# Kernel optimization log

Measured on AMD Instinct MI355X. Metric: run time of the kernel, lower is better.

Reference implementation:

```python
import jax, jax.numpy as jnp
import numpy as np

WS = (2, 7, 7)          # window size (Wd, Wh, Ww)
SS = (1, 3, 3)          # shift size
DIM = 96
HEADS = 3
HD = DIM // HEADS       # head dim = 32
N = WS[0] * WS[1] * WS[2]  # 98 tokens per window
EPS = 1e-5


def _rel_index():
    c = np.stack(np.meshgrid(np.arange(WS[0]), np.arange(WS[1]), np.arange(WS[2]), indexing='ij')).reshape(3, -1)
    r = (c[:, :, None] - c[:, None, :]).transpose(1, 2, 0)  # (N, N, 3)
    r[..., 0] += WS[0] - 1
    r[..., 1] += WS[1] - 1
    r[..., 2] += WS[2] - 1
    r[..., 0] *= (2 * WS[1] - 1) * (2 * WS[2] - 1)
    r[..., 1] *= 2 * WS[2] - 1
    return jnp.asarray(r.sum(-1))  # (N, N) int

REL_IDX = _rel_index()


def _ln(x, w, b):
    m = x.mean(-1, keepdims=True)
    v = ((x - m) ** 2).mean(-1, keepdims=True)
    return (x - m) * jax.lax.rsqrt(v + EPS) * w + b


def setup_inputs() -> dict:
    key = jax.random.key(0)
    ks = jax.random.split(key, 10)
    B, D, H, W, C = 2, 16, 112, 112, DIM
    nW = (D // WS[0]) * (H // WS[1]) * (W // WS[2])  # 2048
    s = 0.02
    tbl = (2 * WS[0] - 1) * (2 * WS[1] - 1) * (2 * WS[2] - 1)
    return dict(
        x=jax.random.normal(ks[0], (B, D, H, W, C), jnp.float32),
        mask=jax.random.normal(ks[1], (nW, N, N), jnp.float32),
        norm1_w=jnp.ones((C,), jnp.float32), norm1_b=jnp.zeros((C,), jnp.float32),
        qkv_w=jax.random.normal(ks[2], (C, 3 * C), jnp.float32) * s,
        qkv_b=jnp.zeros((3 * C,), jnp.float32),
        rpb_table=jax.random.normal(ks[3], (tbl, HEADS), jnp.float32) * s,
        proj_w=jax.random.normal(ks[4], (C, C), jnp.float32) * s,
        proj_b=jnp.zeros((C,), jnp.float32),
        norm2_w=jnp.ones((C,), jnp.float32), norm2_b=jnp.zeros((C,), jnp.float32),
        fc1_w=jax.random.normal(ks[5], (C, 4 * C), jnp.float32) * s,
        fc1_b=jnp.zeros((4 * C,), jnp.float32),
        fc2_w=jax.random.normal(ks[6], (4 * C, C), jnp.float32) * s,
        fc2_b=jnp.zeros((C,), jnp.float32),
    )


def reference(x, mask, norm1_w, norm1_b, qkv_w, qkv_b, rpb_table, proj_w, proj_b,
              norm2_w, norm2_b, fc1_w, fc1_b, fc2_w, fc2_b):
    B, D, H, W, C = x.shape
    shortcut = x
    x = _ln(x, norm1_w, norm1_b)
    # shift (dims divisible by window -> no padding needed)
    x = jnp.roll(x, shift=(-SS[0], -SS[1], -SS[2]), axis=(1, 2, 3))
    nd, nh, nw = D // WS[0], H // WS[1], W // WS[2]
    # window partition -> (B*nW, N, C)
    xw = x.reshape(B, nd, WS[0], nh, WS[1], nw, WS[2], C)
    xw = xw.transpose(0, 1, 3, 5, 2, 4, 6, 7).reshape(-1, N, C)
    B_ = xw.shape[0]
    qkv = (xw @ qkv_w + qkv_b).reshape(B_, N, 3, HEADS, HD).transpose(2, 0, 3, 1, 4)
    q, k, v = qkv[0] * (HD ** -0.5), qkv[1], qkv[2]
    attn = jnp.einsum('bhnd,bhmd->bhnm', q, k)  # (B_, H, N, N)
    bias = rpb_table[REL_IDX.reshape(-1)].reshape(N, N, HEADS).transpose(2, 0, 1)
    attn = attn + bias[None]
    nWm = mask.shape[0]
    attn = attn.reshape(B_ // nWm, nWm, HEADS, N, N) + mask[None, :, None]
    attn = jax.nn.softmax(attn.reshape(B_, HEADS, N, N), axis=-1)
    out = jnp.einsum('bhnm,bhmd->bhnd', attn, v).transpose(0, 2, 1, 3).reshape(B_, N, C)
    out = out @ proj_w + proj_b
    # window reverse
    x = out.reshape(B, nd, nh, nw, WS[0], WS[1], WS[2], C)
    x = x.transpose(0, 1, 4, 2, 5, 3, 6, 7).reshape(B, D, H, W, C)
    x = jnp.roll(x, shift=SS, axis=(1, 2, 3))
    x = shortcut + x
    y = _ln(x, norm2_w, norm2_b)
    y = jax.nn.gelu(y @ fc1_w + fc1_b, approximate=False) @ fc2_w + fc2_b
    return x + y
```

## Files before the change

### kernel.cpp

```cpp
#include <hip/hip_runtime.h>

typedef float f32x4 __attribute__((ext_vector_type(4)));
typedef __bf16 bf16x8 __attribute__((ext_vector_type(8)));
typedef unsigned short ushort_t;
typedef ushort_t us4 __attribute__((ext_vector_type(4)));
typedef unsigned int u32x4 __attribute__((ext_vector_type(4)));

#define MFMA16(a, b, c) __builtin_amdgcn_mfma_f32_16x16x32_bf16((a), (b), (c), 0, 0, 0)

__device__ __forceinline__ ushort_t f2bf(float f) {
    unsigned int u = __builtin_bit_cast(unsigned int, f);
    u += 0x7fffu + ((u >> 16) & 1u);
    return (ushort_t)(u >> 16);
}
__device__ __forceinline__ float bf2f(ushort_t u) {
    return __builtin_bit_cast(float, (unsigned int)u << 16);
}
__device__ __forceinline__ unsigned int packbf2(float lo, float hi) {
    return ((unsigned int)f2bf(hi) << 16) | (unsigned int)f2bf(lo);
}

__device__ __forceinline__ float gelu_fast(float x) {
    float x2 = x * x;
    float t = __builtin_fmaf(0.044715f * x2, x, x);
    float e = __builtin_amdgcn_exp2f(t * (-1.5957691216f * 1.44269504f));
    return x * __builtin_amdgcn_rcpf(1.0f + e);
}

#define NTOK 98
#define CCH 96
#define QSCALE 0.17677669529663687f

#define WQKVP_OFF   ((size_t)0)
#define WPROJP_OFF  (WQKVP_OFF + (size_t)27648 * 2)
#define WFC1P_OFF   (WPROJP_OFF + (size_t)9216 * 2)
#define WFC2P_OFF   (WFC1P_OFF + (size_t)36864 * 2)
#define BIAS2_OFF   (WFC2P_OFF + (size_t)36864 * 2)
#define MASK2_OFF   (BIAS2_OFF + (size_t)37632 * 2 + 256)

__global__ __launch_bounds__(256) void prep_kernel(
    const float* __restrict__ qkv_w, const float* __restrict__ proj_w,
    const float* __restrict__ fc1_w, const float* __restrict__ fc2_w,
    const float* __restrict__ rpb,
    ushort_t* __restrict__ wqkvP, ushort_t* __restrict__ wprojP,
    ushort_t* __restrict__ wfc1P, ushort_t* __restrict__ wfc2P,
    ushort_t* __restrict__ bias2)
{
    int i = blockIdx.x * 256 + threadIdx.x;
    if (i < 27648) {
        int f = i >> 9, r = i & 511, lane = r >> 3, m = r & 7;
        int k0 = f % 3, t = f / 3, nt = t % 2, t2 = t / 2, w = t2 % 3, h = t2 / 3;
        int row = k0 * 32 + (lane >> 4) * 8 + m;
        int col = w * 96 + h * 32 + nt * 16 + (lane & 15);
        wqkvP[i] = f2bf(qkv_w[row * 288 + col]);
        return;
    }
    i -= 27648;
    if (i < 9216) {
        int f = i >> 9, r = i & 511, lane = r >> 3, m = r & 7;
        int k0 = f % 3, nt = f / 3;
        int row = k0 * 32 + (lane >> 4) * 8 + m;
        int col = nt * 16 + (lane & 15);
        wprojP[i] = f2bf(proj_w[row * 96 + col]);
        return;
    }
    i -= 9216;
    if (i < 36864) {
        int f = i >> 9, r = i & 511, lane = r >> 3, m = r & 7;
        int k0 = f % 3, nt = f / 3;
        int row = k0 * 32 + (lane >> 4) * 8 + m;
        int col = nt * 16 + (lane & 15);
        wfc1P[i] = f2bf(fc1_w[row * 384 + col]);
        return;
    }
    i -= 36864;
    if (i < 36864) {
        int f = i >> 9, r = i & 511, lane = r >> 3, m = r & 7;
        int k0 = f % 12, nt = f / 12;
        int row = k0 * 32 + (lane >> 4) * 8 + m;
        int col = nt * 16 + (lane & 15);
        wfc2P[i] = f2bf(fc2_w[row * 96 + col]);
        return;
    }
    i -= 36864;
    if (i < 37632) {
        int h = i / 12544, rem = i % 12544;
        int mt = rem / 1792, rem2 = rem % 1792, kc = rem2 >> 4, r16 = rem2 & 15;
        int row = mt * 16 + r16;
        float v = 0.f;
        if (row < 98 && kc < 98) {
            int rd = row / 49 - kc / 49 + 1;
            int rh = (row % 49) / 7 - (kc % 49) / 7 + 6;
            int rw = row % 7 - kc % 7 + 6;
            v = rpb[((rd * 13 + rh) * 13 + rw) * 3 + h];
        }
        bias2[i] = f2bf(v);
    }
}

__global__ __launch_bounds__(256) void mask2_kernel(
    const float* __restrict__ mask, ushort_t* __restrict__ mask2)
{
    __shared__ float m_lds[9604];
    const int wm = blockIdx.x;
    const float* mw = mask + (size_t)wm * 9604;
    for (int i = threadIdx.x; i < 9604; i += 256) m_lds[i] = mw[i];
    __syncthreads();
    ushort_t* out = mask2 + (size_t)wm * 12544;
    for (int g = threadIdx.x; g < 3136; g += 256) {
        int mt = g / 448, rem = g % 448, kc = rem >> 2, r4 = (rem & 3) * 4;
        us4 o;
        #pragma unroll
        for (int e = 0; e < 4; ++e) {
            int row = mt * 16 + r4 + e;
            float v = (row < 98 && kc < 98) ? m_lds[row * 98 + kc] : -1e30f;
            o[e] = f2bf(v);
        }
        *(us4*)(out + (size_t)g * 4) = o;
    }
}

__global__ __launch_bounds__(192, 3) void fused_attn(
    const float* __restrict__ x, const ushort_t* __restrict__ mask2,
    const float* __restrict__ n1w, const float* __restrict__ n1b,
    const float* __restrict__ qkv_b, const float* __restrict__ proj_b,
    const ushort_t* __restrict__ wqkvP, const ushort_t* __restrict__ wprojP,
    const ushort_t* __restrict__ bias2, float* __restrict__ dout)
{
    __shared__ ushort_t xw_lds[112 * 104];
    __shared__ ushort_t sc_all[3][2176];
    __shared__ int tokbase[112];

    const int tid  = threadIdx.x;
    const int lane = tid & 63;
    const int wave = tid >> 6;
    const int l16  = lane & 15, lg = lane >> 4;

    const int b  = blockIdx.x;
    const int wm = (b & 7) * 256 + ((b >> 3) >> 1);
    const int bb = (b >> 3) & 1;
    const int id_ = wm >> 8, ih = (wm >> 4) & 15, iw = wm & 15;

    if (tid < 98) {
        int td = tid / 49, r49 = tid - td * 49, th = r49 / 7, tw = r49 - th * 7;
        int od = (id_ * 2 + td + 1) & 15;
        int oh = ih * 7 + th + 3; if (oh >= 112) oh -= 112;
        int ow = iw * 7 + tw + 3; if (ow >= 112) ow -= 112;
        tokbase[tid] = ((((bb << 4) + od) * 112 + oh) * 112 + ow) * 96;
    }
    {
        us4 z4 = {0, 0, 0, 0};
        for (int i = tid; i < 14 * 26; i += 192) {
            int t = 98 + i / 26, c4 = (i % 26) * 4;
            *(us4*)(xw_lds + t * 104 + c4) = z4;
        }
    }
    __syncthreads();

    {
        const int g = tid >> 5, lane32 = tid & 31;
        for (int t = g; t < 98; t += 6) {
            const float* xp = x + tokbase[t];
            float v0 = xp[lane32], v1 = xp[lane32 + 32], v2 = xp[lane32 + 64];
            float s = v0 + v1 + v2, sq = v0 * v0 + v1 * v1 + v2 * v2;
            #pragma unroll
            for (int m = 1; m < 32; m <<= 1) { s += __shfl_xor(s, m); sq += __shfl_xor(sq, m); }
            float mean = s * (1.0f / 96.0f);
            float var = sq * (1.0f / 96.0f) - mean * mean;
            float rs = rsqrtf(var + 1e-5f);
            ushort_t* op = xw_lds + t * 104;
            op[lane32]      = f2bf((v0 - mean) * rs * n1w[lane32]      + n1b[lane32]);
            op[lane32 + 32] = f2bf((v1 - mean) * rs * n1w[lane32 + 32] + n1b[lane32 + 32]);
            op[lane32 + 64] = f2bf((v2 - mean) * rs * n1w[lane32 + 64] + n1b[lane32 + 64]);
        }
    }
    __syncthreads();

    const int h = wave;
    ushort_t* sc = sc_all[wave];
    const ushort_t* m2w = mask2 + (size_t)wm * 12544;
    const ushort_t* b2h = bias2 + (size_t)h * 12544;

    bf16x8 qf[7], kf[7], vf[2][4];

    #pragma unroll
    for (int which = 0; which < 2; ++which) {
        bf16x8 bw[2][3];
        float  bia[2];
        #pragma unroll
        for (int nt = 0; nt < 2; ++nt) {
            bia[nt] = qkv_b[which * 96 + h * 32 + nt * 16 + l16];
            #pragma unroll
            for (int k0 = 0; k0 < 3; ++k0)
                bw[nt][k0] = *(const bf16x8*)(wqkvP + ((((h * 3 + which) * 2 + nt) * 3 + k0) << 9) + lane * 8);
        }
        for (int mt = 0; mt < 7; ++mt) {
            const ushort_t* ap = xw_lds + (mt * 16 + l16) * 104 + lg * 8;
            bf16x8 a0 = *(const bf16x8*)(ap);
            bf16x8 a1 = *(const bf16x8*)(ap + 32);
            bf16x8 a2 = *(const bf16x8*)(ap + 64);
            #pragma unroll
            for (int nt = 0; nt < 2; ++nt) {
                f32x4 acc = {0.f, 0.f, 0.f, 0.f};
                acc = MFMA16(a0, bw[nt][0], acc);
                acc = MFMA16(a1, bw[nt][1], acc);
                acc = MFMA16(a2, bw[nt][2], acc);
                float scl = (which == 0) ? QSCALE : 1.0f;
                #pragma unroll
                for (int j = 0; j < 4; ++j)
                    sc[(lg * 4 + j) * 36 + nt * 16 + l16] = f2bf((acc[j] + bia[nt]) * scl);
            }
            if (which == 0) qf[mt] = *(const bf16x8*)(sc + l16 * 36 + lg * 8);
            else            kf[mt] = *(const bf16x8*)(sc + l16 * 36 + lg * 8);
        }
    }

    {
        bf16x8 bw[2][3];
        float  bia[2];
        #pragma unroll
        for (int nt = 0; nt < 2; ++nt) {
            bia[nt] = qkv_b[192 + h * 32 + nt * 16 + l16];
            #pragma unroll
            for (int k0 = 0; k0 < 3; ++k0)
                bw[nt][k0] = *(const bf16x8*)(wqkvP + ((((h * 3 + 2) * 2 + nt) * 3 + k0) << 9) + lane * 8);
        }
        #pragma unroll
        for (int k0 = 0; k0 < 4; ++k0) {
            unsigned int pkv[2][2][2];
            #pragma unroll
            for (int half = 0; half < 2; ++half) {
                int mtp = 2 * k0 + half;
                if (mtp < 7) {
                    const ushort_t* ap = xw_lds + (mtp * 16 + l16) * 104 + lg * 8;
                    bf16x8 a0 = *(const bf16x8*)(ap);
                    bf16x8 a1 = *(const bf16x8*)(ap + 32);
                    bf16x8 a2 = *(const bf16x8*)(ap + 64);
                    #pragma unroll
                    for (int nt2 = 0; nt2 < 2; ++nt2) {
                        f32x4 acc = {0.f, 0.f, 0.f, 0.f};
                        acc = MFMA16(a0, bw[nt2][0], acc);
                        acc = MFMA16(a1, bw[nt2][1], acc);
                        acc = MFMA16(a2, bw[nt2][2], acc);
                        pkv[half][nt2][0] = packbf2(acc[0] + bia[nt2], acc[1] + bia[nt2]);
                        pkv[half][nt2][1] = packbf2(acc[2] + bia[nt2], acc[3] + bia[nt2]);
                    }
                } else {
                    pkv[half][0][0] = pkv[half][0][1] = 0u;
                    pkv[half][1][0] = pkv[half][1][1] = 0u;
                }
            }
            #pragma unroll
            for (int nt2 = 0; nt2 < 2; ++nt2) {
                u32x4 w;
                #pragma unroll
                for (int e = 0; e < 4; ++e) {
                    int s = l16 + 16 * (2 * (lg & 1) + (e >> 1));
                    unsigned int t0 = (unsigned int)__shfl((int)pkv[0][nt2][e & 1], s, 64);
                    unsigned int t1 = (unsigned int)__shfl((int)pkv[1][nt2][e & 1], s, 64);
                    w[e] = (lg >> 1) ? t1 : t0;
                }
                vf[nt2][k0] = __builtin_bit_cast(bf16x8, w);
            }
        }
    }
    __syncthreads();

    ushort_t* out = xw_lds;

    if (lane < 32) {
        us4 z4 = {0, 0, 0, 0};
        *(us4*)(sc + (lane >> 1) * 136 + 112 + (lane & 1) * 8) = z4;
        *(us4*)(sc + (lane >> 1) * 136 + 116 + (lane & 1) * 8) = z4;
    }

    #pragma unroll
    for (int mt = 0; mt < 7; ++mt) {
        const ushort_t* m2t = m2w + mt * 1792;
        const ushort_t* b2t = b2h + mt * 1792;
        us4 mv[7];
        #pragma unroll
        for (int nt = 0; nt < 7; ++nt)
            mv[nt] = *(const us4*)(m2t + (nt * 16 + l16) * 16 + lg * 4);

        f32x4 sums = {0.f, 0.f, 0.f, 0.f};
        #pragma unroll
        for (int nt = 0; nt < 7; ++nt) {
            us4 bv = *(const us4*)(b2t + (nt * 16 + l16) * 16 + lg * 4);
            f32x4 z = {0.f, 0.f, 0.f, 0.f};
            f32x4 stv = MFMA16(qf[mt], kf[nt], z);
            #pragma unroll
            for (int j = 0; j < 4; ++j) {
                float e_ = __expf(stv[j] + bf2f(mv[nt][j]) + bf2f(bv[j]));
                sums[j] += e_;
                sc[(lg * 4 + j) * 136 + nt * 16 + l16] = f2bf(e_);
            }
        }
        f32x4 inv;
        #pragma unroll
        for (int j = 0; j < 4; ++j) {
            float s = sums[j];
            s += __shfl_xor(s, 1); s += __shfl_xor(s, 2);
            s += __shfl_xor(s, 4); s += __shfl_xor(s, 8);
            inv[j] = __builtin_amdgcn_rcpf(s);
        }
        bf16x8 pf[4];
        #pragma unroll
        for (int k0 = 0; k0 < 4; ++k0)
            pf[k0] = *(const bf16x8*)(sc + l16 * 136 + k0 * 32 + lg * 8);
        #pragma unroll
        for (int nt2 = 0; nt2 < 2; ++nt2) {
            f32x4 acc = {0.f, 0.f, 0.f, 0.f};
            #pragma unroll
            for (int k0 = 0; k0 < 4; ++k0) acc = MFMA16(pf[k0], vf[nt2][k0], acc);
            #pragma unroll
            for (int j = 0; j < 4; ++j) {
                int tok = mt * 16 + lg * 4 + j;
                if (tok < 98)
                    out[tok * 104 + h * 32 + nt2 * 16 + l16] = f2bf(acc[j] * inv[j]);
            }
        }
    }
    __syncthreads();

    for (int job = wave; job < 42; job += 3) {
        int mt = job / 6, nt = job % 6;
        int cg = nt * 16 + l16;
        f32x4 acc = {0.f, 0.f, 0.f, 0.f};
        #pragma unroll
        for (int k0 = 0; k0 < 3; ++k0) {
            bf16x8 ao = *(const bf16x8*)(out + (mt * 16 + l16) * 104 + k0 * 32 + lg * 8);
            bf16x8 bp = *(const bf16x8*)(wprojP + ((nt * 3 + k0) << 9) + lane * 8);
            acc = MFMA16(ao, bp, acc);
        }
        float pb = proj_b[cg];
        #pragma unroll
        for (int j = 0; j < 4; ++j) {
            int tok = mt * 16 + lg * 4 + j;
            if (tok < 98) {
                int g = tokbase[tok] + cg;
                dout[g] = x[g] + acc[j] + pb;
            }
        }
    }
}

__global__ __launch_bounds__(512, 2) void mlp_kernel(
    float* __restrict__ xres, const float* __restrict__ w2, const float* __restrict__ b2,
    const ushort_t* __restrict__ wfc1P, const float* __restrict__ fc1_b,
    const ushort_t* __restrict__ wfc2P, const float* __restrict__ fc2_b)
{
    __shared__ ushort_t A_ln[64 * 104];
    __shared__ ushort_t h_lds[64 * 392];
    const int tid = threadIdx.x;
    const int lane = tid & 63, wave = tid >> 6;
    const int l16 = lane & 15, lg = lane >> 4;
    const size_t t0 = (size_t)blockIdx.x * 64;

    {
        int t = tid >> 3, sub = tid & 7;
        const float* xp = xres + (t0 + t) * 96;
        f32x4 v[3];
        float s = 0.f, sq = 0.f;
        #pragma unroll
        for (int j4 = 0; j4 < 3; ++j4) {
            v[j4] = *(const f32x4*)(xp + (j4 * 8 + sub) * 4);
            #pragma unroll
            for (int e = 0; e < 4; ++e) { s += v[j4][e]; sq += v[j4][e] * v[j4][e]; }
        }
        s += __shfl_xor(s, 1); s += __shfl_xor(s, 2); s += __shfl_xor(s, 4);
        sq += __shfl_xor(sq, 1); sq += __shfl_xor(sq, 2); sq += __shfl_xor(sq, 4);
        float mean = s * (1.0f / 96.0f);
        float var = sq * (1.0f / 96.0f) - mean * mean;
        float rs = rsqrtf(var + 1e-5f);
        #pragma unroll
        for (int j4 = 0; j4 < 3; ++j4) {
            int c0 = (j4 * 8 + sub) * 4;
            us4 pk;
            #pragma unroll
            for (int e = 0; e < 4; ++e)
                pk[e] = f2bf((v[j4][e] - mean) * rs * w2[c0 + e] + b2[c0 + e]);
            *(us4*)(A_ln + t * 104 + c0) = pk;
        }
    }
    __syncthreads();

    for (int job = wave; job < 96; job += 8) {
        int mt = job / 24, nt = job % 24;
        int n = nt * 16 + l16;
        f32x4 acc = {0.f, 0.f, 0.f, 0.f};
        #pragma unroll
        for (int k0 = 0; k0 < 3; ++k0) {
            bf16x8 a  = *(const bf16x8*)(A_ln + (mt * 16 + l16) * 104 + k0 * 32 + lg * 8);
            bf16x8 bw = *(const bf16x8*)(wfc1P + ((nt * 3 + k0) << 9) + lane * 8);
            acc = MFMA16(a, bw, acc);
        }
        float bv = fc1_b[n];
        #pragma unroll
        for (int j = 0; j < 4; ++j) {
            int tok = mt * 16 + lg * 4 + j;
            h_lds[tok * 392 + n] = f2bf(gelu_fast(acc[j] + bv));
        }
    }
    __syncthreads();

    for (int job = wave; job < 24; job += 8) {
        int mt = job / 6, nt = job % 6;
        int c = nt * 16 + l16;
        f32x4 acc = {0.f, 0.f, 0.f, 0.f};
        #pragma unroll
        for (int k0 = 0; k0 < 12; ++k0) {
            bf16x8 a  = *(const bf16x8*)(h_lds + (mt * 16 + l16) * 392 + k0 * 32 + lg * 8);
            bf16x8 bw = *(const bf16x8*)(wfc2P + ((nt * 12 + k0) << 9) + lane * 8);
            acc = MFMA16(a, bw, acc);
        }
        float bv = fc2_b[c];
        #pragma unroll
        for (int j = 0; j < 4; ++j) {
            int tok = mt * 16 + lg * 4 + j;
            size_t g = (t0 + tok) * 96 + c;
            xres[g] = xres[g] + acc[j] + bv;
        }
    }
}

extern "C" void kernel_launch(void* const* d_in, const int* in_sizes, int n_in,
                              void* d_out, int out_size, void* d_ws, size_t ws_size,
                              hipStream_t stream) {
    const float* x      = (const float*)d_in[0];
    const float* mask   = (const float*)d_in[1];
    const float* n1w    = (const float*)d_in[2];
    const float* n1b    = (const float*)d_in[3];
    const float* qkv_w  = (const float*)d_in[4];
    const float* qkv_b  = (const float*)d_in[5];
    const float* rpb    = (const float*)d_in[6];
    const float* proj_w = (const float*)d_in[7];
    const float* proj_b = (const float*)d_in[8];
    const float* n2w    = (const float*)d_in[9];
    const float* n2b    = (const float*)d_in[10];
    const float* fc1_w  = (const float*)d_in[11];
    const float* fc1_b  = (const float*)d_in[12];
    const float* fc2_w  = (const float*)d_in[13];
    const float* fc2_b  = (const float*)d_in[14];

    char* ws = (char*)d_ws;
    ushort_t* wqkvP  = (ushort_t*)(ws + WQKVP_OFF);
    ushort_t* wprojP = (ushort_t*)(ws + WPROJP_OFF);
    ushort_t* wfc1P  = (ushort_t*)(ws + WFC1P_OFF);
    ushort_t* wfc2P  = (ushort_t*)(ws + WFC2P_OFF);
    ushort_t* bias2  = (ushort_t*)(ws + BIAS2_OFF);
    ushort_t* mask2  = (ushort_t*)(ws + MASK2_OFF);
    float*    dout   = (float*)d_out;

    prep_kernel<<<579, 256, 0, stream>>>(qkv_w, proj_w, fc1_w, fc2_w, rpb,
                                         wqkvP, wprojP, wfc1P, wfc2P, bias2);
    mask2_kernel<<<2048, 256, 0, stream>>>(mask, mask2);
    fused_attn<<<4096, 192, 0, stream>>>(x, mask2, n1w, n1b, qkv_b, proj_b,
                                         wqkvP, wprojP, bias2, dout);
    mlp_kernel<<<6272, 512, 0, stream>>>(dout, n2w, n2b, wfc1P, fc1_b, wfc2P, fc2_b);
}
```

Measured before the change: 504.4 us.

## Interleave score exponentiation with PV MFMAs in 32-column chunks

Restructures the per-row-tile attention loop so that scores are computed, exponentiated and written to a small 16x32 LDS staging buffer two column tiles at a time, then immediately consumed by the P·V MFMAs. The staging buffer shrinks from 16x136 to 16x36 per wave, which reduces LDS footprint and may improve occupancy or shorten live ranges. Mask and bias loads are issued per tile instead of being prefetched as a group. The cost is more LDS round trips and dependencies inside the loop, which could leave less room for latency hiding.

```diff
diff --git a/kernel.cpp b/kernel.cpp
--- a/kernel.cpp
+++ b/kernel.cpp
@@ -128,7 +128,7 @@
     const ushort_t* __restrict__ bias2, float* __restrict__ dout)
 {
     __shared__ ushort_t xw_lds[112 * 104];
-    __shared__ ushort_t sc_all[3][2176];
+    __shared__ ushort_t sc_all[3][576];
     __shared__ int tokbase[112];
 
     const int tid  = threadIdx.x;
@@ -268,33 +268,39 @@
 
     ushort_t* out = xw_lds;
 
-    if (lane < 32) {
-        us4 z4 = {0, 0, 0, 0};
-        *(us4*)(sc + (lane >> 1) * 136 + 112 + (lane & 1) * 8) = z4;
-        *(us4*)(sc + (lane >> 1) * 136 + 116 + (lane & 1) * 8) = z4;
-    }
-
     #pragma unroll
     for (int mt = 0; mt < 7; ++mt) {
         const ushort_t* m2t = m2w + mt * 1792;
         const ushort_t* b2t = b2h + mt * 1792;
-        us4 mv[7];
-        #pragma unroll
-        for (int nt = 0; nt < 7; ++nt)
-            mv[nt] = *(const us4*)(m2t + (nt * 16 + l16) * 16 + lg * 4);
 
         f32x4 sums = {0.f, 0.f, 0.f, 0.f};
-        #pragma unroll
-        for (int nt = 0; nt < 7; ++nt) {
-            us4 bv = *(const us4*)(b2t + (nt * 16 + l16) * 16 + lg * 4);
-            f32x4 z = {0.f, 0.f, 0.f, 0.f};
-            f32x4 stv = MFMA16(qf[mt], kf[nt], z);
-            #pragma unroll
-            for (int j = 0; j < 4; ++j) {
-                float e_ = __expf(stv[j] + bf2f(mv[nt][j]) + bf2f(bv[j]));
-                sums[j] += e_;
-                sc[(lg * 4 + j) * 136 + nt * 16 + l16] = f2bf(e_);
-            }
+        f32x4 oacc0 = {0.f, 0.f, 0.f, 0.f};
+        f32x4 oacc1 = {0.f, 0.f, 0.f, 0.f};
+        #pragma unroll
+        for (int c = 0; c < 4; ++c) {
+            #pragma unroll
+            for (int ntl = 0; ntl < 2; ++ntl) {
+                const int nt = 2 * c + ntl;
+                if (nt < 7) {
+                    us4 mv = *(const us4*)(m2t + (nt * 16 + l16) * 16 + lg * 4);
+                    us4 bv = *(const us4*)(b2t + (nt * 16 + l16) * 16 + lg * 4);
+                    f32x4 z = {0.f, 0.f, 0.f, 0.f};
+                    f32x4 stv = MFMA16(qf[mt], kf[nt], z);
+                    #pragma unroll
+                    for (int j = 0; j < 4; ++j) {
+                        float e_ = __expf(stv[j] + bf2f(mv[j]) + bf2f(bv[j]));
+                        sums[j] += e_;
+                        sc[(lg * 4 + j) * 36 + ntl * 16 + l16] = f2bf(e_);
+                    }
+                } else {
+                    #pragma unroll
+                    for (int j = 0; j < 4; ++j)
+                        sc[(lg * 4 + j) * 36 + 16 + l16] = 0;
+                }
+            }
+            bf16x8 pf = *(const bf16x8*)(sc + l16 * 36 + lg * 8);
+            oacc0 = MFMA16(pf, vf[0][c], oacc0);
+            oacc1 = MFMA16(pf, vf[1][c], oacc1);
         }
         f32x4 inv;
         #pragma unroll
@@ -304,20 +310,12 @@
             s += __shfl_xor(s, 4); s += __shfl_xor(s, 8);
             inv[j] = __builtin_amdgcn_rcpf(s);
         }
-        bf16x8 pf[4];
-        #pragma unroll
-        for (int k0 = 0; k0 < 4; ++k0)
-            pf[k0] = *(const bf16x8*)(sc + l16 * 136 + k0 * 32 + lg * 8);
-        #pragma unroll
-        for (int nt2 = 0; nt2 < 2; ++nt2) {
-            f32x4 acc = {0.f, 0.f, 0.f, 0.f};
-            #pragma unroll
-            for (int k0 = 0; k0 < 4; ++k0) acc = MFMA16(pf[k0], vf[nt2][k0], acc);
-            #pragma unroll
-            for (int j = 0; j < 4; ++j) {
-                int tok = mt * 16 + lg * 4 + j;
-                if (tok < 98)
-                    out[tok * 104 + h * 32 + nt2 * 16 + l16] = f2bf(acc[j] * inv[j]);
+        #pragma unroll
+        for (int j = 0; j < 4; ++j) {
+            int tok = mt * 16 + lg * 4 + j;
+            if (tok < 98) {
+                out[tok * 104 + h * 32 + l16]      = f2bf(oacc0[j] * inv[j]);
+                out[tok * 104 + h * 32 + 16 + l16] = f2bf(oacc1[j] * inv[j]);
             }
         }
     }
```

Result: slower. 591.7 us (+17.3%).
